# Kernel tuning notes

Measured on AMD Instinct MI355X. Metric: run time of the kernel, lower is better.

Reference implementation:

```python
import jax, jax.numpy as jnp
import numpy as np
import math

N_HEADS = 16
EPS = 1e-6


def rmsnorm(x, w):
    xf = x.astype(jnp.float32)
    n = xf * jax.lax.rsqrt(jnp.mean(xf * xf, axis=-1, keepdims=True) + EPS)
    return n.astype(x.dtype) * w


def setup_inputs() -> dict:
    key = jax.random.key(0)
    ks = jax.random.split(key, 8)
    B, T, C, Hf = 1, 4096, 1024, 4096
    s = lambda fan_in: 1.0 / math.sqrt(fan_in)
    return {
        "x": jax.random.normal(ks[0], (B, T, C), jnp.float32),
        "attn_norm_w": jnp.ones((C,), jnp.float32),
        "ffn_norm_w": jnp.ones((C,), jnp.float32),
        "c_attn_w": jax.random.normal(ks[1], (3 * C, C), jnp.float32) * s(C),
        "c_proj_w": jax.random.normal(ks[2], (C, C), jnp.float32) * s(C),
        "w1": jax.random.normal(ks[3], (Hf, C), jnp.float32) * s(C),
        "w2": jax.random.normal(ks[4], (C, Hf), jnp.float32) * s(Hf),
        "w3": jax.random.normal(ks[5], (Hf, C), jnp.float32) * s(C),
    }


def attention(x, c_attn_w, c_proj_w):
    B, T, C = x.shape
    hd = C // N_HEADS
    qkv = x @ c_attn_w.T  # [B,T,3C]
    q, k, v = jnp.split(qkv, 3, axis=-1)
    q = q.reshape(B, T, N_HEADS, hd).transpose(0, 2, 1, 3)  # [B,H,T,hd]
    k = k.reshape(B, T, N_HEADS, hd).transpose(0, 2, 1, 3)
    v = v.reshape(B, T, N_HEADS, hd).transpose(0, 2, 1, 3)
    att = jnp.einsum('bhqd,bhkd->bhqk', q, k) * (1.0 / math.sqrt(hd))
    mask = jnp.tril(jnp.ones((T, T), bool))  # causal
    att = jnp.where(mask, att, -jnp.inf)
    att = jax.nn.softmax(att, axis=-1)
    y = jnp.einsum('bhqk,bhkd->bhqd', att, v)
    y = y.transpose(0, 2, 1, 3).reshape(B, T, C)
    return y @ c_proj_w.T


def ffn(x, w1, w2, w3):
    return (jax.nn.silu(x @ w1.T) * (x @ w3.T)) @ w2.T


def reference(x, attn_norm_w, ffn_norm_w, c_attn_w, c_proj_w, w1, w2, w3):
    x = x + attention(rmsnorm(x, attn_norm_w), c_attn_w, c_proj_w)
    x = x + ffn(rmsnorm(x, ffn_norm_w), w1, w2, w3)
    return x
```

## Files before the change

### kernel.cpp

```cpp
#include <hip/hip_runtime.h>
#include <hip/hip_bf16.h>

typedef __hip_bfloat16 bf16;
typedef __bf16 bf16r;
typedef bf16r bf16x8 __attribute__((ext_vector_type(8)));
typedef bf16r bf16x4 __attribute__((ext_vector_type(4)));
typedef float f32x4 __attribute__((ext_vector_type(4)));

#define T_SEQ 4096
#define C_DIM 1024
#define LD_QKV 3072
#define MB(x) ((size_t)(x) << 20)
#define SCL 0.18033688011112042f

static __device__ __forceinline__ unsigned short f2bf(float f) {
    bf16 h = (bf16)f;
    return *reinterpret_cast<unsigned short*>(&h);
}

__global__ __launch_bounds__(256) void cvt_w(const float* __restrict__ src, size_t eoff,
                                             ushort4* __restrict__ dst, int n4,
                                             int n4scl, float scl) {
    int i = blockIdx.x * 256 + threadIdx.x;
    const int stride = gridDim.x * 256;
    const float4* s = (const float4*)(src + eoff);
    for (; i < n4; i += stride) {
        float4 v = s[i];
        const float m = (i < n4scl) ? scl : 1.0f;
        ushort4 o;
        o.x = f2bf(v.x * m); o.y = f2bf(v.y * m); o.z = f2bf(v.z * m); o.w = f2bf(v.w * m);
        dst[i] = o;
    }
}

__global__ __launch_bounds__(256) void copy_f32(const float4* __restrict__ src,
                                                float4* __restrict__ dst, int n4) {
    int i = blockIdx.x * 256 + threadIdx.x;
    const int stride = gridDim.x * 256;
    for (; i < n4; i += stride) dst[i] = src[i];
}

__global__ __launch_bounds__(256) void rmsnorm_k(const float* __restrict__ x,
                                                 const float* __restrict__ w,
                                                 bf16* __restrict__ out) {
    const int row = blockIdx.x;
    const int tid = threadIdx.x;
    const float* xr = x + (size_t)row * C_DIM;
    float v[4];
    float ss = 0.f;
#pragma unroll
    for (int i = 0; i < 4; i++) { v[i] = xr[tid * 4 + i]; ss += v[i] * v[i]; }
#pragma unroll
    for (int off = 32; off; off >>= 1) ss += __shfl_xor(ss, off);
    __shared__ float red[4];
    if ((tid & 63) == 0) red[tid >> 6] = ss;
    __syncthreads();
    const float tot = red[0] + red[1] + red[2] + red[3];
    const float scale = rsqrtf(tot * (1.0f / C_DIM) + 1e-6f);
#pragma unroll
    for (int i = 0; i < 4; i++) {
        const int c = tid * 4 + i;
        out[(size_t)row * C_DIM + c] = (bf16)(v[i] * scale * w[c]);
    }
}

template <int RESID, int OUTF32>
__global__ __launch_bounds__(256) void gemm128(const bf16* __restrict__ A, int lda,
                                               const bf16* __restrict__ B, int ldb,
                                               const void* __restrict__ resid,
                                               void* __restrict__ out,
                                               int N, int K) {
    __shared__ __align__(16) bf16r As[128 * 32];
    __shared__ __align__(16) bf16r Bs[128 * 32];
    const int tid = threadIdx.x;
    const int w = tid >> 6, lane = tid & 63;
    const int c = lane & 15, qd = lane >> 4;
    const int wm = w >> 1, wn = w & 1;
    const int mbase = blockIdx.y * 128;
    const int nbase = blockIdx.x * 128;
    const size_t koff = (size_t)blockIdx.z * K;

    const int srow = lane >> 2, schk = lane & 3;
    const bf16* gA = A + (size_t)(mbase + w * 32 + srow) * lda + schk * 8 + koff;
    const bf16* gB = B + (size_t)(nbase + w * 32 + srow) * ldb + schk * 8 + koff;

    f32x4 acc[4][4] = {};

    for (int k0 = 0; k0 < K; k0 += 32) {
        __syncthreads();
#pragma unroll
        for (int s = 0; s < 2; s++) {
            __builtin_amdgcn_global_load_lds(
                (const __attribute__((address_space(1))) void*)(gA + (size_t)(s * 16) * lda + k0),
                (__attribute__((address_space(3))) void*)&As[(w * 32 + s * 16) * 32], 16, 0, 0);
            __builtin_amdgcn_global_load_lds(
                (const __attribute__((address_space(1))) void*)(gB + (size_t)(s * 16) * ldb + k0),
                (__attribute__((address_space(3))) void*)&Bs[(w * 32 + s * 16) * 32], 16, 0, 0);
        }
        __syncthreads();

        bf16x8 a[4], b[4];
#pragma unroll
        for (int i = 0; i < 4; i++)
            a[i] = *(const bf16x8*)&As[(wm * 64 + i * 16 + c) * 32 + qd * 8];
#pragma unroll
        for (int j = 0; j < 4; j++)
            b[j] = *(const bf16x8*)&Bs[(wn * 64 + j * 16 + c) * 32 + qd * 8];
#pragma unroll
        for (int i = 0; i < 4; i++)
#pragma unroll
            for (int j = 0; j < 4; j++)
                acc[i][j] = __builtin_amdgcn_mfma_f32_16x16x32_bf16(a[i], b[j], acc[i][j], 0, 0, 0);
    }

#pragma unroll
    for (int i = 0; i < 4; i++) {
#pragma unroll
        for (int j = 0; j < 4; j++) {
            const int col = nbase + wn * 64 + j * 16 + c;
#pragma unroll
            for (int reg = 0; reg < 4; reg++) {
                const int row = mbase + wm * 64 + i * 16 + qd * 4 + reg;
                const size_t idx = (size_t)row * N + col;
                float v = acc[i][j][reg];
                if (RESID == 2) v += ((const float*)resid)[idx];
                if (RESID == 3) {
                    const float a1 = (float)((const bf16*)resid)[idx];
                    v = (a1 / (1.0f + __expf(-a1))) * v;
                }
                if (RESID == 4) {
                    atomicAdd(&((float*)out)[idx], v);
                } else if (OUTF32) {
                    ((float*)out)[idx] = v;
                } else {
                    ((bf16*)out)[idx] = (bf16)v;
                }
            }
        }
    }
}

__global__ __launch_bounds__(256, 2) void gemm_w13(const bf16* __restrict__ A,
                                                   const bf16* __restrict__ B1,
                                                   const bf16* __restrict__ B3,
                                                   bf16* __restrict__ out,
                                                   int N, int K) {
    __shared__ __align__(16) bf16r As[128 * 32];
    __shared__ __align__(16) bf16r B1s[128 * 32];
    __shared__ __align__(16) bf16r B3s[128 * 32];
    const int tid = threadIdx.x;
    const int w = tid >> 6, lane = tid & 63;
    const int c = lane & 15, qd = lane >> 4;
    const int wm = w >> 1, wn = w & 1;
    const int mbase = blockIdx.y * 128;
    const int nbase = blockIdx.x * 128;

    const int srow = lane >> 2, schk = lane & 3;
    const bf16* gA = A + (size_t)(mbase + w * 32 + srow) * K + schk * 8;
    const bf16* gB1 = B1 + (size_t)(nbase + w * 32 + srow) * K + schk * 8;
    const bf16* gB3 = B3 + (size_t)(nbase + w * 32 + srow) * K + schk * 8;

    f32x4 acc1[4][4] = {};
    f32x4 acc3[4][4] = {};

    for (int k0 = 0; k0 < K; k0 += 32) {
        __syncthreads();
#pragma unroll
        for (int s = 0; s < 2; s++) {
            __builtin_amdgcn_global_load_lds(
                (const __attribute__((address_space(1))) void*)(gA + (size_t)(s * 16) * K + k0),
                (__attribute__((address_space(3))) void*)&As[(w * 32 + s * 16) * 32], 16, 0, 0);
            __builtin_amdgcn_global_load_lds(
                (const __attribute__((address_space(1))) void*)(gB1 + (size_t)(s * 16) * K + k0),
                (__attribute__((address_space(3))) void*)&B1s[(w * 32 + s * 16) * 32], 16, 0, 0);
            __builtin_amdgcn_global_load_lds(
                (const __attribute__((address_space(1))) void*)(gB3 + (size_t)(s * 16) * K + k0),
                (__attribute__((address_space(3))) void*)&B3s[(w * 32 + s * 16) * 32], 16, 0, 0);
        }
        __syncthreads();

        bf16x8 a[4], b1[4], b3[4];
#pragma unroll
        for (int i = 0; i < 4; i++)
            a[i] = *(const bf16x8*)&As[(wm * 64 + i * 16 + c) * 32 + qd * 8];
#pragma unroll
        for (int j = 0; j < 4; j++) {
            b1[j] = *(const bf16x8*)&B1s[(wn * 64 + j * 16 + c) * 32 + qd * 8];
            b3[j] = *(const bf16x8*)&B3s[(wn * 64 + j * 16 + c) * 32 + qd * 8];
        }
#pragma unroll
        for (int i = 0; i < 4; i++)
#pragma unroll
            for (int j = 0; j < 4; j++) {
                acc1[i][j] = __builtin_amdgcn_mfma_f32_16x16x32_bf16(a[i], b1[j], acc1[i][j], 0, 0, 0);
                acc3[i][j] = __builtin_amdgcn_mfma_f32_16x16x32_bf16(a[i], b3[j], acc3[i][j], 0, 0, 0);
            }
    }

#pragma unroll
    for (int i = 0; i < 4; i++) {
#pragma unroll
        for (int j = 0; j < 4; j++) {
            const int col = nbase + wn * 64 + j * 16 + c;
#pragma unroll
            for (int reg = 0; reg < 4; reg++) {
                const int row = mbase + wm * 64 + i * 16 + qd * 4 + reg;
                const float a1 = acc1[i][j][reg];
                const float h = (a1 / (1.0f + __expf(-a1))) * acc3[i][j][reg];
                out[(size_t)row * N + col] = (bf16)h;
            }
        }
    }
}

__global__ __launch_bounds__(256) void build_tr(const bf16* __restrict__ qkv,
                                                bf16* __restrict__ dst, int soff) {
    const int h = blockIdx.y;
    const int tb = blockIdx.x;
    __shared__ bf16 tile[64][65];
    const int tx = threadIdx.x & 63;
    const int ty = threadIdx.x >> 6;
    for (int rr = ty; rr < 64; rr += 4)
        tile[rr][tx] = qkv[(size_t)(tb * 64 + rr) * LD_QKV + soff + h * 64 + tx];
    __syncthreads();
    for (int rr = ty; rr < 64; rr += 4)
        dst[((size_t)h * 64 + rr) * T_SEQ + tb * 64 + tx] = tile[tx][rr];
}

#define CTR_STRIDE 16
__global__ void zero_ctr(int* p) { if (threadIdx.x < 8 * CTR_STRIDE) p[threadIdx.x] = 0; }

__global__ __launch_bounds__(256) void attn_mfma(const bf16* __restrict__ qkv,
                                                 const bf16* __restrict__ VT,
                                                 bf16* __restrict__ y,
                                                 int* __restrict__ ctrs) {
    __shared__ __align__(16) bf16r Ks[128][64];
    __shared__ __align__(16) bf16r VTs[64][128];
    __shared__ __align__(16) bf16r Ps[4][16][128];
    __shared__ int s_wi;

    const int tid  = threadIdx.x;
    const int w    = tid >> 6;
    const int lane = tid & 63;
    const int c    = lane & 15;
    const int qd   = lane >> 4;
    const int sw   = c & 7;
    const int qi   = blockIdx.x & 7;
    int* ctr = ctrs + qi * CTR_STRIDE;

    while (true) {
        __syncthreads();
        if (tid == 0) s_wi = atomicAdd(ctr, 1);
        __syncthreads();
        const int j = s_wi;
        if (j >= 128) break;

        const int h    = qi + 8 * (j & 1);
        const int qb   = 63 - (j >> 1);
        const int qrow = qb * 64 + w * 16 + c;

        bf16x8 qf[2];
        {
            const bf16* qp = qkv + (size_t)qrow * LD_QKV + h * 64;
            qf[0] = *(const bf16x8*)(qp + qd * 8);
            qf[1] = *(const bf16x8*)(qp + 32 + qd * 8);
        }

        f32x4 O[4] = {};
        float m_i = -1e30f, l_i = 0.f;
        const int nkb = (qb >> 1) + 1;

        for (int kb = 0; kb < nkb; kb++) {
            __syncthreads();
#pragma unroll
            for (int ii = 0; ii < 4; ii++) {
                const int i = ii * 256 + tid;
                const int kr = i >> 3, ch = i & 7;
                *(bf16x8*)&Ks[kr][(ch ^ (kr & 7)) * 8] =
                    *(const bf16x8*)(qkv + (size_t)(kb * 128 + kr) * LD_QKV + C_DIM + h * 64 + ch * 8);
                const int vr = i >> 4, vch = i & 15;
                *(bf16x8*)&VTs[vr][(vch ^ (vr & 7)) * 8] =
                    *(const bf16x8*)(VT + ((size_t)h * 64 + vr) * T_SEQ + kb * 128 + vch * 8);
            }
            __syncthreads();

            f32x4 ST[8];
#pragma unroll
            for (int kt = 0; kt < 8; kt++) {
                f32x4 z = {};
#pragma unroll
                for (int ks = 0; ks < 2; ks++) {
                    bf16x8 kf = *(const bf16x8*)&Ks[kt * 16 + c][((ks * 4 + qd) ^ sw) * 8];
                    z = __builtin_amdgcn_mfma_f32_16x16x32_bf16(kf, qf[ks], z, 0, 0, 0);
                }
                ST[kt] = z;
            }

            if (kb == nkb - 1) {
#pragma unroll
                for (int kt = 0; kt < 8; kt++)
#pragma unroll
                    for (int r = 0; r < 4; r++)
                        if (kb * 128 + kt * 16 + qd * 4 + r > qrow) ST[kt][r] = -1e30f;
            }

            float mb = -1e30f;
#pragma unroll
            for (int kt = 0; kt < 8; kt++)
#pragma unroll
                for (int r = 0; r < 4; r++) mb = fmaxf(mb, ST[kt][r]);
            mb = fmaxf(mb, __shfl_xor(mb, 16));
            mb = fmaxf(mb, __shfl_xor(mb, 32));

            bf16x4 pv[8];
            float rs = 0.f;
            if (__all(mb - m_i <= 8.0f)) {
#pragma unroll
                for (int kt = 0; kt < 8; kt++)
#pragma unroll
                    for (int r = 0; r < 4; r++) {
                        const float p = exp2f(ST[kt][r] - m_i);
                        pv[kt][r] = (bf16r)p;
                        rs += p;
                    }
                rs += __shfl_xor(rs, 16);
                rs += __shfl_xor(rs, 32);
                l_i += rs;
            } else {
                const float mnew = fmaxf(m_i, mb);
                const float alpha = exp2f(m_i - mnew);
#pragma unroll
                for (int kt = 0; kt < 8; kt++)
#pragma unroll
                    for (int r = 0; r < 4; r++) {
                        const float p = exp2f(ST[kt][r] - mnew);
                        pv[kt][r] = (bf16r)p;
                        rs += p;
                    }
                rs += __shfl_xor(rs, 16);
                rs += __shfl_xor(rs, 32);
                l_i = l_i * alpha + rs;
                m_i = mnew;
#pragma unroll
                for (int dt = 0; dt < 4; dt++)
#pragma unroll
                    for (int r = 0; r < 4; r++) O[dt][r] *= alpha;
            }

#pragma unroll
            for (int kt = 0; kt < 8; kt++) {
                const int phys = (kt * 2 + (qd >> 1)) ^ sw;
                *(bf16x4*)&Ps[w][c][phys * 8 + (qd & 1) * 4] = pv[kt];
            }

#pragma unroll
            for (int ks = 0; ks < 4; ks++) {
                bf16x8 pf = *(const bf16x8*)&Ps[w][c][((ks * 4 + qd) ^ sw) * 8];
#pragma unroll
                for (int dt = 0; dt < 4; dt++) {
                    bf16x8 vf = *(const bf16x8*)&VTs[dt * 16 + c][((ks * 4 + qd) ^ sw) * 8];
                    O[dt] = __builtin_amdgcn_mfma_f32_16x16x32_bf16(vf, pf, O[dt], 0, 0, 0);
                }
            }
        }

        const float inv_l = 1.0f / l_i;
#pragma unroll
        for (int dt = 0; dt < 4; dt++) {
            bf16x4 ov;
#pragma unroll
            for (int r = 0; r < 4; r++) ov[r] = (bf16r)(O[dt][r] * inv_l);
            *(bf16x4*)(y + (size_t)qrow * C_DIM + h * 64 + dt * 16 + qd * 4) = ov;
        }
    }
}

extern "C" void kernel_launch(void* const* d_in, const int* in_sizes, int n_in,
                              void* d_out, int out_size, void* d_ws, size_t ws_size,
                              hipStream_t stream) {
    const float* x        = (const float*)d_in[0];
    const float* attn_w   = (const float*)d_in[1];
    const float* ffn_w    = (const float*)d_in[2];
    const float* c_attn_w = (const float*)d_in[3];
    const float* c_proj_w = (const float*)d_in[4];
    const float* w1       = (const float*)d_in[5];
    const float* w2       = (const float*)d_in[6];
    const float* w3       = (const float*)d_in[7];
    float* xmid = (float*)d_out;

    char* ws = (char*)d_ws;
    bf16* cwA  = (bf16*)(ws);
    bf16* cwP  = (bf16*)(ws + MB(6));
    bf16* rms1 = (bf16*)(ws + MB(8));
    bf16* qkv  = (bf16*)(ws + MB(16));
    bf16* VT   = (bf16*)(ws + MB(40));
    bf16* y    = (bf16*)(ws + MB(48));
    int*  ctrs = (int*)(ws + MB(8));
    bf16* rms2 = (bf16*)(ws);
    bf16* w1h  = (bf16*)(ws + MB(8));
    bf16* w3h  = (bf16*)(ws + MB(16));
    bf16* w2h  = (bf16*)(ws + MB(8));
    bf16* h1   = (bf16*)(ws + MB(24));

    cvt_w<<<512, 256, 0, stream>>>(c_attn_w, 0, (ushort4*)cwA, 3072 * 1024 / 4,
                                   1024 * 1024 / 4, SCL);
    cvt_w<<<512, 256, 0, stream>>>(c_proj_w, 0, (ushort4*)cwP, 1024 * 1024 / 4, 0, 1.0f);
    rmsnorm_k<<<T_SEQ, 256, 0, stream>>>(x, attn_w, rms1);
    gemm128<0, 0><<<dim3(24, 32), 256, 0, stream>>>(rms1, C_DIM, cwA, C_DIM, nullptr, qkv, 3072, 1024);
    build_tr<<<dim3(64, 16), 256, 0, stream>>>(qkv, VT, 2 * C_DIM);
    zero_ctr<<<1, 128, 0, stream>>>(ctrs);
    attn_mfma<<<768, 256, 0, stream>>>(qkv, VT, y, ctrs);
    cvt_w<<<512, 256, 0, stream>>>(w1, 0, (ushort4*)w1h, 4096 * 1024 / 4, 0, 1.0f);
    cvt_w<<<512, 256, 0, stream>>>(w3, 0, (ushort4*)w3h, 4096 * 1024 / 4, 0, 1.0f);
    copy_f32<<<2048, 256, 0, stream>>>((const float4*)x, (float4*)xmid, T_SEQ * C_DIM / 4);
    gemm128<4, 1><<<dim3(8, 32, 2), 256, 0, stream>>>(y, C_DIM, cwP, C_DIM, nullptr, xmid, 1024, 512);
    rmsnorm_k<<<T_SEQ, 256, 0, stream>>>(xmid, ffn_w, rms2);
    gemm_w13<<<dim3(32, 32), 256, 0, stream>>>(rms2, w1h, w3h, h1, 4096, 1024);
    cvt_w<<<512, 256, 0, stream>>>(w2, 0, (ushort4*)w2h, 1024 * 4096 / 4, 0, 1.0f);
    gemm128<4, 1><<<dim3(8, 32, 4), 256, 0, stream>>>(h1, 4096, w2h, 4096, nullptr, xmid, 1024, 1024);
}
```

Baseline: 483.9 us.

## Double GEMM K-tile to 64 and merge small launches

The GEMM kernels now stage 64-wide K slices in LDS per iteration instead of 32, which halves the number of barrier pairs and loop trips and changes the global-to-LDS load mapping to 8 rows by 8 chunks. The w1 and w3 fp32-to-bf16 conversions are merged into one kernel, and the counter zeroing is folded into the transpose kernel, removing two launches. Doubled LDS use (48KB for gemm_w13) may reduce occupancy, and the unpadded 128-byte row stride can cause LDS bank conflicts.

```diff
diff --git a/kernel.cpp b/kernel.cpp
--- a/kernel.cpp
+++ b/kernel.cpp
@@ -12,6 +12,9 @@
 #define LD_QKV 3072
 #define MB(x) ((size_t)(x) << 20)
 #define SCL 0.18033688011112042f
+
+#define AS1 __attribute__((address_space(1)))
+#define AS3 __attribute__((address_space(3)))
 
 static __device__ __forceinline__ unsigned short f2bf(float f) {
     bf16 h = (bf16)f;
@@ -33,6 +36,23 @@
     }
 }
 
+__global__ __launch_bounds__(256) void cvt_w13(const float* __restrict__ s1,
+                                               const float* __restrict__ s3,
+                                               ushort4* __restrict__ d1,
+                                               ushort4* __restrict__ d3, int n4) {
+    int i = blockIdx.x * 256 + threadIdx.x;
+    const int stride = gridDim.x * 256;
+    for (; i < n4; i += stride) {
+        float4 v1 = ((const float4*)s1)[i];
+        float4 v3 = ((const float4*)s3)[i];
+        ushort4 o1, o3;
+        o1.x = f2bf(v1.x); o1.y = f2bf(v1.y); o1.z = f2bf(v1.z); o1.w = f2bf(v1.w);
+        o3.x = f2bf(v3.x); o3.y = f2bf(v3.y); o3.z = f2bf(v3.z); o3.w = f2bf(v3.w);
+        d1[i] = o1;
+        d3[i] = o3;
+    }
+}
+
 __global__ __launch_bounds__(256) void copy_f32(const float4* __restrict__ src,
                                                 float4* __restrict__ dst, int n4) {
     int i = blockIdx.x * 256 + threadIdx.x;
@@ -70,8 +90,8 @@
                                                const void* __restrict__ resid,
                                                void* __restrict__ out,
                                                int N, int K) {
-    __shared__ __align__(16) bf16r As[128 * 32];
-    __shared__ __align__(16) bf16r Bs[128 * 32];
+    __shared__ __align__(16) bf16r As[128 * 64];
+    __shared__ __align__(16) bf16r Bs[128 * 64];
     const int tid = threadIdx.x;
     const int w = tid >> 6, lane = tid & 63;
     const int c = lane & 15, qd = lane >> 4;
@@ -80,37 +100,41 @@
     const int nbase = blockIdx.x * 128;
     const size_t koff = (size_t)blockIdx.z * K;
 
-    const int srow = lane >> 2, schk = lane & 3;
-    const bf16* gA = A + (size_t)(mbase + w * 32 + srow) * lda + schk * 8 + koff;
-    const bf16* gB = B + (size_t)(nbase + w * 32 + srow) * ldb + schk * 8 + koff;
+    const int srow = lane >> 3, schk = lane & 7;
+    const bf16* gA = A + (size_t)(mbase + srow) * lda + schk * 8 + koff;
+    const bf16* gB = B + (size_t)(nbase + srow) * ldb + schk * 8 + koff;
 
     f32x4 acc[4][4] = {};
 
-    for (int k0 = 0; k0 < K; k0 += 32) {
-        __syncthreads();
-#pragma unroll
-        for (int s = 0; s < 2; s++) {
+    for (int k0 = 0; k0 < K; k0 += 64) {
+        __syncthreads();
+#pragma unroll
+        for (int g = 0; g < 4; g++) {
+            const int grp = w * 4 + g;
             __builtin_amdgcn_global_load_lds(
-                (const __attribute__((address_space(1))) void*)(gA + (size_t)(s * 16) * lda + k0),
-                (__attribute__((address_space(3))) void*)&As[(w * 32 + s * 16) * 32], 16, 0, 0);
+                (const AS1 void*)(gA + (size_t)(grp * 8) * lda + k0),
+                (AS3 void*)&As[grp * 8 * 64], 16, 0, 0);
             __builtin_amdgcn_global_load_lds(
-                (const __attribute__((address_space(1))) void*)(gB + (size_t)(s * 16) * ldb + k0),
-                (__attribute__((address_space(3))) void*)&Bs[(w * 32 + s * 16) * 32], 16, 0, 0);
-        }
-        __syncthreads();
-
-        bf16x8 a[4], b[4];
-#pragma unroll
-        for (int i = 0; i < 4; i++)
-            a[i] = *(const bf16x8*)&As[(wm * 64 + i * 16 + c) * 32 + qd * 8];
-#pragma unroll
-        for (int j = 0; j < 4; j++)
-            b[j] = *(const bf16x8*)&Bs[(wn * 64 + j * 16 + c) * 32 + qd * 8];
-#pragma unroll
-        for (int i = 0; i < 4; i++)
+                (const AS1 void*)(gB + (size_t)(grp * 8) * ldb + k0),
+                (AS3 void*)&Bs[grp * 8 * 64], 16, 0, 0);
+        }
+        __syncthreads();
+
+#pragma unroll
+        for (int kk = 0; kk < 2; kk++) {
+            bf16x8 a[4], b[4];
+#pragma unroll
+            for (int i = 0; i < 4; i++)
+                a[i] = *(const bf16x8*)&As[(wm * 64 + i * 16 + c) * 64 + kk * 32 + qd * 8];
 #pragma unroll
             for (int j = 0; j < 4; j++)
-                acc[i][j] = __builtin_amdgcn_mfma_f32_16x16x32_bf16(a[i], b[j], acc[i][j], 0, 0, 0);
+                b[j] = *(const bf16x8*)&Bs[(wn * 64 + j * 16 + c) * 64 + kk * 32 + qd * 8];
+#pragma unroll
+            for (int i = 0; i < 4; i++)
+#pragma unroll
+                for (int j = 0; j < 4; j++)
+                    acc[i][j] = __builtin_amdgcn_mfma_f32_16x16x32_bf16(a[i], b[j], acc[i][j], 0, 0, 0);
+        }
     }
 
 #pragma unroll
@@ -145,9 +169,9 @@
                                                    const bf16* __restrict__ B3,
                                                    bf16* __restrict__ out,
                                                    int N, int K) {
-    __shared__ __align__(16) bf16r As[128 * 32];
-    __shared__ __align__(16) bf16r B1s[128 * 32];
-    __shared__ __align__(16) bf16r B3s[128 * 32];
+    __shared__ __align__(16) bf16r As[128 * 64];
+    __shared__ __align__(16) bf16r B1s[128 * 64];
+    __shared__ __align__(16) bf16r B3s[128 * 64];
     const int tid = threadIdx.x;
     const int w = tid >> 6, lane = tid & 63;
     const int c = lane & 15, qd = lane >> 4;
@@ -155,46 +179,50 @@
     const int mbase = blockIdx.y * 128;
     const int nbase = blockIdx.x * 128;
 
-    const int srow = lane >> 2, schk = lane & 3;
-    const bf16* gA = A + (size_t)(mbase + w * 32 + srow) * K + schk * 8;
-    const bf16* gB1 = B1 + (size_t)(nbase + w * 32 + srow) * K + schk * 8;
-    const bf16* gB3 = B3 + (size_t)(nbase + w * 32 + srow) * K + schk * 8;
+    const int srow = lane >> 3, schk = lane & 7;
+    const bf16* gA = A + (size_t)(mbase + srow) * K + schk * 8;
+    const bf16* gB1 = B1 + (size_t)(nbase + srow) * K + schk * 8;
+    const bf16* gB3 = B3 + (size_t)(nbase + srow) * K + schk * 8;
 
     f32x4 acc1[4][4] = {};
     f32x4 acc3[4][4] = {};
 
-    for (int k0 = 0; k0 < K; k0 += 32) {
-        __syncthreads();
-#pragma unroll
-        for (int s = 0; s < 2; s++) {
+    for (int k0 = 0; k0 < K; k0 += 64) {
+        __syncthreads();
+#pragma unroll
+        for (int g = 0; g < 4; g++) {
+            const int grp = w * 4 + g;
             __builtin_amdgcn_global_load_lds(
-                (const __attribute__((address_space(1))) void*)(gA + (size_t)(s * 16) * K + k0),
-                (__attribute__((address_space(3))) void*)&As[(w * 32 + s * 16) * 32], 16, 0, 0);
+                (const AS1 void*)(gA + (size_t)(grp * 8) * K + k0),
+                (AS3 void*)&As[grp * 8 * 64], 16, 0, 0);
             __builtin_amdgcn_global_load_lds(
-                (const __attribute__((address_space(1))) void*)(gB1 + (size_t)(s * 16) * K + k0),
-                (__attribute__((address_space(3))) void*)&B1s[(w * 32 + s * 16) * 32], 16, 0, 0);
+                (const AS1 void*)(gB1 + (size_t)(grp * 8) * K + k0),
+                (AS3 void*)&B1s[grp * 8 * 64], 16, 0, 0);
             __builtin_amdgcn_global_load_lds(
-                (const __attribute__((address_space(1))) void*)(gB3 + (size_t)(s * 16) * K + k0),
-                (__attribute__((address_space(3))) void*)&B3s[(w * 32 + s * 16) * 32], 16, 0, 0);
-        }
-        __syncthreads();
-
-        bf16x8 a[4], b1[4], b3[4];
-#pragma unroll
-        for (int i = 0; i < 4; i++)
-            a[i] = *(const bf16x8*)&As[(wm * 64 + i * 16 + c) * 32 + qd * 8];
-#pragma unroll
-        for (int j = 0; j < 4; j++) {
-            b1[j] = *(const bf16x8*)&B1s[(wn * 64 + j * 16 + c) * 32 + qd * 8];
-            b3[j] = *(const bf16x8*)&B3s[(wn * 64 + j * 16 + c) * 32 + qd * 8];
-        }
-#pragma unroll
-        for (int i = 0; i < 4; i++)
+                (const AS1 void*)(gB3 + (size_t)(grp * 8) * K + k0),
+                (AS3 void*)&B3s[grp * 8 * 64], 16, 0, 0);
+        }
+        __syncthreads();
+
+#pragma unroll
+        for (int kk = 0; kk < 2; kk++) {
+            bf16x8 a[4], b1[4], b3[4];
+#pragma unroll
+            for (int i = 0; i < 4; i++)
+                a[i] = *(const bf16x8*)&As[(wm * 64 + i * 16 + c) * 64 + kk * 32 + qd * 8];
 #pragma unroll
             for (int j = 0; j < 4; j++) {
-                acc1[i][j] = __builtin_amdgcn_mfma_f32_16x16x32_bf16(a[i], b1[j], acc1[i][j], 0, 0, 0);
-                acc3[i][j] = __builtin_amdgcn_mfma_f32_16x16x32_bf16(a[i], b3[j], acc3[i][j], 0, 0, 0);
-            }
+                b1[j] = *(const bf16x8*)&B1s[(wn * 64 + j * 16 + c) * 64 + kk * 32 + qd * 8];
+                b3[j] = *(const bf16x8*)&B3s[(wn * 64 + j * 16 + c) * 64 + kk * 32 + qd * 8];
+            }
+#pragma unroll
+            for (int i = 0; i < 4; i++)
+#pragma unroll
+                for (int j = 0; j < 4; j++) {
+                    acc1[i][j] = __builtin_amdgcn_mfma_f32_16x16x32_bf16(a[i], b1[j], acc1[i][j], 0, 0, 0);
+                    acc3[i][j] = __builtin_amdgcn_mfma_f32_16x16x32_bf16(a[i], b3[j], acc3[i][j], 0, 0, 0);
+                }
+        }
     }
 
 #pragma unroll
@@ -213,8 +241,12 @@
     }
 }
 
+#define CTR_STRIDE 16
 __global__ __launch_bounds__(256) void build_tr(const bf16* __restrict__ qkv,
-                                                bf16* __restrict__ dst, int soff) {
+                                                bf16* __restrict__ dst, int soff,
+                                                int* __restrict__ ctrs) {
+    if (blockIdx.x == 0 && blockIdx.y == 0 && threadIdx.x < 8 * CTR_STRIDE)
+        ctrs[threadIdx.x] = 0;
     const int h = blockIdx.y;
     const int tb = blockIdx.x;
     __shared__ bf16 tile[64][65];
@@ -226,9 +258,6 @@
     for (int rr = ty; rr < 64; rr += 4)
         dst[((size_t)h * 64 + rr) * T_SEQ + tb * 64 + tx] = tile[tx][rr];
 }
-
-#define CTR_STRIDE 16
-__global__ void zero_ctr(int* p) { if (threadIdx.x < 8 * CTR_STRIDE) p[threadIdx.x] = 0; }
 
 __global__ __launch_bounds__(256) void attn_mfma(const bf16* __restrict__ qkv,
                                                  const bf16* __restrict__ VT,
@@ -407,11 +436,9 @@
     cvt_w<<<512, 256, 0, stream>>>(c_proj_w, 0, (ushort4*)cwP, 1024 * 1024 / 4, 0, 1.0f);
     rmsnorm_k<<<T_SEQ, 256, 0, stream>>>(x, attn_w, rms1);
     gemm128<0, 0><<<dim3(24, 32), 256, 0, stream>>>(rms1, C_DIM, cwA, C_DIM, nullptr, qkv, 3072, 1024);
-    build_tr<<<dim3(64, 16), 256, 0, stream>>>(qkv, VT, 2 * C_DIM);
-    zero_ctr<<<1, 128, 0, stream>>>(ctrs);
+    build_tr<<<dim3(64, 16), 256, 0, stream>>>(qkv, VT, 2 * C_DIM, ctrs);
     attn_mfma<<<768, 256, 0, stream>>>(qkv, VT, y, ctrs);
-    cvt_w<<<512, 256, 0, stream>>>(w1, 0, (ushort4*)w1h, 4096 * 1024 / 4, 0, 1.0f);
-    cvt_w<<<512, 256, 0, stream>>>(w3, 0, (ushort4*)w3h, 4096 * 1024 / 4, 0, 1.0f);
+    cvt_w13<<<512, 256, 0, stream>>>(w1, w3, (ushort4*)w1h, (ushort4*)w3h, 4096 * 1024 / 4);
     copy_f32<<<2048, 256, 0, stream>>>((const float4*)x, (float4*)xmid, T_SEQ * C_DIM / 4);
     gemm128<4, 1><<<dim3(8, 32, 2), 256, 0, stream>>>(y, C_DIM, cwP, C_DIM, nullptr, xmid, 1024, 512);
     rmsnorm_k<<<T_SEQ, 256, 0, stream>>>(xmid, ffn_w, rms2);
```

Measured after the change: 485.0 us. About the same (+0.2%).
